# Kernel tuning notes

Measured on AMD Instinct MI355X. Metric: run time of the kernel, lower is better.

## Reference

```python
import jax, jax.numpy as jnp
import numpy as np

N, DIN, DOUT, R, E = 100000, 128, 256, 4, 600000
EPS = 1e-12


def setup_inputs() -> dict:
    key = jax.random.key(0)
    ks = jax.random.split(key, 8)
    x = jax.random.normal(ks[0], (N, DIN), dtype=jnp.float32)
    edge_index = jax.random.randint(ks[1], (R, 2, E), 0, N, dtype=jnp.int32)
    s1 = 1.0 / np.sqrt(DIN)
    s2 = 1.0 / np.sqrt(DOUT)
    W1n = jax.random.uniform(ks[2], (R, DOUT, DIN), jnp.float32, -s1, s1)
    W1r = jax.random.uniform(ks[3], (R, DOUT, DIN), jnp.float32, -s1, s1)
    b1 = jnp.zeros((R, DOUT), jnp.float32)
    W2n = jax.random.uniform(ks[4], (R, DOUT, DOUT), jnp.float32, -s2, s2)
    W2r = jax.random.uniform(ks[5], (R, DOUT, DOUT), jnp.float32, -s2, s2)
    b2 = jnp.zeros((R, DOUT), jnp.float32)
    return {"x": x, "edge_index": edge_index, "W1n": W1n, "b1": b1,
            "W1r": W1r, "W2n": W2n, "b2": b2, "W2r": W2r}


def _hetero_sage_layer(x, edge_index, Wn, b, Wr):
    # per-relation sum-aggregate of source features into destinations: [R, N, D]
    agg = jax.vmap(
        lambda e: jax.ops.segment_sum(x[e[0]], e[1], num_segments=N)
    )(edge_index)
    # SAGEConv: lin_l(agg) + bias + lin_r(x); mean across relations (to_hetero aggr='mean')
    out = (jnp.einsum('rnd,rod->rno', agg, Wn)
           + b[:, None, :]
           + jnp.einsum('nd,rod->rno', x, Wr))
    return out.mean(axis=0)  # [N, DOUT]


def _l2_normalize(h):
    nrm = jnp.sqrt(jnp.sum(h * h, axis=-1, keepdims=True))
    return h / jnp.maximum(nrm, EPS)


def reference(x, edge_index, W1n, b1, W1r, W2n, b2, W2r):
    h = _hetero_sage_layer(x, edge_index, W1n, b1, W1r)
    h = jax.nn.relu(_l2_normalize(h))  # dropout is identity in eval mode
    out = _hetero_sage_layer(h, edge_index, W2n, b2, W2r)
    return out  # x_dict['note']
```

## Files before the change

### kernel.cpp

```cpp
#include <hip/hip_runtime.h>
#include <hip/hip_bf16.h>

#define NN 100000
#define DIN 128
#define DOUT 256
#define RR 4
#define EE 600000
#define NB (RR * NN)
#define SCAN_BLKS 400
#define SCAN_CHUNK 1000
#define PBLKS 2048

typedef __attribute__((ext_vector_type(4))) float f32x4;
typedef __attribute__((ext_vector_type(8))) short short8;
typedef __attribute__((ext_vector_type(2))) uint uint2v;

__device__ __forceinline__ float bf2f(ushort u) {
    union { unsigned int i; float f; } v; v.i = ((unsigned int)u) << 16; return v.f;
}
__device__ __forceinline__ ushort f2bf(float f) {
    union { float f; unsigned int i; } v; v.f = f;
    unsigned int r = v.i + 0x7fff + ((v.i >> 16) & 1);
    return (ushort)(r >> 16);
}

__device__ __forceinline__ void ld_g2l16(const void* g, void* l) {
    __builtin_amdgcn_global_load_lds(
        (const __attribute__((address_space(1))) void*)g,
        (__attribute__((address_space(3))) void*)l, 16, 0, 0);
}

__device__ __forceinline__ void store_w(ushort* W, int kd, int o, float s) {
    int cs = ((kd >> 3) & 7) ^ (o & 7);
    W[((size_t)(kd >> 6) * 256 + o) * 64 + cs * 8 + (kd & 7)] = f2bf(s);
}

#define W1ELEMS (5 * 128 * 256)
#define W2ELEMS (5 * 256 * 256)
__global__ void wprep_all(const float* __restrict__ W1n, const float* __restrict__ W1r,
                          const float* __restrict__ W2n, const float* __restrict__ W2r,
                          const float* __restrict__ b1, const float* __restrict__ b2,
                          ushort* __restrict__ W1c, ushort* __restrict__ W2c,
                          float* __restrict__ b1s, float* __restrict__ b2s) {
    int idx = blockIdx.x * blockDim.x + threadIdx.x;
    if (idx < W1ELEMS) {
        int p = idx / (128 * 256), rem = idx - p * (128 * 256);
        int k = rem >> 8, o = rem & 255;
        float s;
        if (p == 0) {
            s = 0.f;
            for (int r = 0; r < RR; ++r) s += W1r[(size_t)r * DOUT * DIN + (long)o * DIN + k];
        } else {
            s = W1n[(size_t)(p - 1) * DOUT * DIN + (long)o * DIN + k];
        }
        store_w(W1c, p * 128 + k, o, s * 0.25f);
        return;
    }
    idx -= W1ELEMS;
    if (idx < W2ELEMS) {
        int p = idx / (256 * 256), rem = idx - p * (256 * 256);
        int k = rem >> 8, o = rem & 255;
        float s;
        if (p == 0) {
            s = 0.f;
            for (int r = 0; r < RR; ++r) s += W2r[(size_t)r * DOUT * DOUT + (long)o * DOUT + k];
        } else {
            s = W2n[(size_t)(p - 1) * DOUT * DOUT + (long)o * DOUT + k];
        }
        store_w(W2c, p * 256 + k, o, s * 0.25f);
        return;
    }
    idx -= W2ELEMS;
    if (idx < 512) {
        int o = idx & 255;
        const float* b = (idx < 256) ? b1 : b2;
        float s = 0.f;
        for (int r = 0; r < RR; ++r) s += b[(long)r * 256 + o];
        ((idx < 256) ? b1s : b2s)[o] = s * 0.25f;
    }
}

__global__ __launch_bounds__(256) void deg_count(const int* __restrict__ ei,
                                                 int* __restrict__ deg) {
    const int CH = EE / 4;
    int p = blockIdx.x & 7;
    const int stride = (PBLKS / 8) * 256;
    for (int idx = (blockIdx.x >> 3) * 256 + threadIdx.x; idx < RR * CH; idx += stride) {
        int r = idx / CH, j = idx - r * CH;
        int4 d = ((const int4*)(ei + (size_t)r * 2 * EE + EE))[j];
        if (((d.x >> 8) & 7) == p) atomicAdd(&deg[r * NN + d.x], 1);
        if (((d.y >> 8) & 7) == p) atomicAdd(&deg[r * NN + d.y], 1);
        if (((d.z >> 8) & 7) == p) atomicAdd(&deg[r * NN + d.z], 1);
        if (((d.w >> 8) & 7) == p) atomicAdd(&deg[r * NN + d.w], 1);
    }
}

__global__ __launch_bounds__(256) void fill_csr(const int* __restrict__ ei,
                                                int* __restrict__ cursor,
                                                int* __restrict__ elist) {
    const int CH = EE / 4;
    int p = blockIdx.x & 7;
    const int stride = (PBLKS / 8) * 256;
    for (int idx = (blockIdx.x >> 3) * 256 + threadIdx.x; idx < RR * CH; idx += stride) {
        int r = idx / CH, j = idx - r * CH;
        int4 d = ((const int4*)(ei + (size_t)r * 2 * EE + EE))[j];
        int4 s = ((const int4*)(ei + (size_t)r * 2 * EE))[j];
        if (((d.x >> 8) & 7) == p) elist[atomicAdd(&cursor[r * NN + d.x], 1)] = s.x;
        if (((d.y >> 8) & 7) == p) elist[atomicAdd(&cursor[r * NN + d.y], 1)] = s.y;
        if (((d.z >> 8) & 7) == p) elist[atomicAdd(&cursor[r * NN + d.z], 1)] = s.z;
        if (((d.w >> 8) & 7) == p) elist[atomicAdd(&cursor[r * NN + d.w], 1)] = s.w;
    }
}

__global__ __launch_bounds__(256) void scan_part(const int* __restrict__ deg,
                                                 int* __restrict__ bsum) {
    int b = blockIdx.x, t = threadIdx.x;
    int s = 0;
    for (int i = t; i < SCAN_CHUNK; i += 256) s += deg[b * SCAN_CHUNK + i];
    for (int o = 32; o > 0; o >>= 1) s += __shfl_down(s, o);
    __shared__ int red[4];
    if ((t & 63) == 0) red[t >> 6] = s;
    __syncthreads();
    if (t == 0) bsum[b] = red[0] + red[1] + red[2] + red[3];
}

__global__ __launch_bounds__(512) void scan_top(int* __restrict__ bsum) {
    __shared__ int v[512];
    int t = threadIdx.x;
    v[t] = (t < SCAN_BLKS) ? bsum[t] : 0;
    __syncthreads();
    for (int st = 1; st < 512; st <<= 1) {
        int tmp = (t >= st) ? v[t - st] : 0;
        __syncthreads();
        v[t] += tmp;
        __syncthreads();
    }
    if (t < SCAN_BLKS) bsum[t] = (t == 0) ? 0 : v[t - 1];
}

__global__ __launch_bounds__(256) void scan_final(int* __restrict__ degc,
                                                  const int* __restrict__ bsum,
                                                  int* __restrict__ off) {
    __shared__ int lv[1024];
    __shared__ int ts[256];
    int b = blockIdx.x, t = threadIdx.x;
    for (int i = t; i < 1024; i += 256)
        lv[i] = (i < SCAN_CHUNK) ? degc[b * SCAN_CHUNK + i] : 0;
    __syncthreads();
    int i0 = t * 4;
    int v0 = lv[i0], v1 = lv[i0 + 1], v2 = lv[i0 + 2], v3 = lv[i0 + 3];
    ts[t] = v0 + v1 + v2 + v3;
    __syncthreads();
    for (int st = 1; st < 256; st <<= 1) {
        int tmp = (t >= st) ? ts[t - st] : 0;
        __syncthreads();
        ts[t] += tmp;
        __syncthreads();
    }
    int run = bsum[b] + (t ? ts[t - 1] : 0);
    if (i0 < SCAN_CHUNK) {
        int base = b * SCAN_CHUNK + i0;
        off[base + 0] = run; degc[base + 0] = run; run += v0;
        off[base + 1] = run; degc[base + 1] = run; run += v1;
        off[base + 2] = run; degc[base + 2] = run; run += v2;
        off[base + 3] = run; degc[base + 3] = run; run += v3;
    }
    if (b == SCAN_BLKS - 1 && t == 255) off[NB] = bsum[b] + ts[255];
}

__global__ void cvt_x(const float* __restrict__ x, ushort* __restrict__ XB) {
    int t = blockIdx.x * blockDim.x + threadIdx.x;
    if (t >= NN * 32) return;
    int n = t >> 5, c4 = (t & 31) * 4;
    float4 v = *(const float4*)&x[(size_t)n * 128 + c4];
    ushort4 o = {f2bf(v.x), f2bf(v.y), f2bf(v.z), f2bf(v.w)};
    *(ushort4*)&XB[(size_t)n * 128 + c4] = o;
}

template <int D>
__global__ void gather_bf16(const ushort* __restrict__ feat,
                            const int* __restrict__ elist, const int* __restrict__ off,
                            ushort* __restrict__ agg, int sout, int chunk) {
    constexpr int V = D / 64;
    int wv = blockIdx.x * 4 + (threadIdx.x >> 6);
    int lane = threadIdx.x & 63;
    if (wv >= NN * chunk) return;
    int n = wv / chunk, rl = wv - n * chunk;
    int b = rl * NN + n;
    int beg = __builtin_amdgcn_readfirstlane(off[b]);
    int end = __builtin_amdgcn_readfirstlane(off[b + 1]);
    float acc[V];
#pragma unroll
    for (int v = 0; v < V; ++v) acc[v] = 0.f;
    const ushort* fbase = feat + lane * V;
    int e = beg;
    for (; e + 4 <= end; e += 4) {
        int s0 = elist[e], s1 = elist[e + 1], s2 = elist[e + 2], s3 = elist[e + 3];
        if constexpr (V == 2) {
            ushort2 a0 = *(const ushort2*)(fbase + (size_t)s0 * D);
            ushort2 a1 = *(const ushort2*)(fbase + (size_t)s1 * D);
            ushort2 a2 = *(const ushort2*)(fbase + (size_t)s2 * D);
            ushort2 a3 = *(const ushort2*)(fbase + (size_t)s3 * D);
            acc[0] += (bf2f(a0.x) + bf2f(a1.x)) + (bf2f(a2.x) + bf2f(a3.x));
            acc[1] += (bf2f(a0.y) + bf2f(a1.y)) + (bf2f(a2.y) + bf2f(a3.y));
        } else {
            ushort4 a0 = *(const ushort4*)(fbase + (size_t)s0 * D);
            ushort4 a1 = *(const ushort4*)(fbase + (size_t)s1 * D);
            ushort4 a2 = *(const ushort4*)(fbase + (size_t)s2 * D);
            ushort4 a3 = *(const ushort4*)(fbase + (size_t)s3 * D);
            acc[0] += (bf2f(a0.x) + bf2f(a1.x)) + (bf2f(a2.x) + bf2f(a3.x));
            acc[1] += (bf2f(a0.y) + bf2f(a1.y)) + (bf2f(a2.y) + bf2f(a3.y));
            acc[2] += (bf2f(a0.z) + bf2f(a1.z)) + (bf2f(a2.z) + bf2f(a3.z));
            acc[3] += (bf2f(a0.w) + bf2f(a1.w)) + (bf2f(a2.w) + bf2f(a3.w));
        }
    }
    for (; e < end; ++e) {
        int s0 = elist[e];
        if constexpr (V == 2) {
            ushort2 a = *(const ushort2*)(fbase + (size_t)s0 * D);
            acc[0] += bf2f(a.x); acc[1] += bf2f(a.y);
        } else {
            ushort4 a = *(const ushort4*)(fbase + (size_t)s0 * D);
            acc[0] += bf2f(a.x); acc[1] += bf2f(a.y);
            acc[2] += bf2f(a.z); acc[3] += bf2f(a.w);
        }
    }
    ushort* op = agg + (size_t)n * sout + rl * D + lane * V;
    if constexpr (V == 2) {
        uint u = (uint)f2bf(acc[0]) | ((uint)f2bf(acc[1]) << 16);
        *(uint*)op = u;
    } else {
        uint2v u;
        u.x = (uint)f2bf(acc[0]) | ((uint)f2bf(acc[1]) << 16);
        u.y = (uint)f2bf(acc[2]) | ((uint)f2bf(acc[3]) << 16);
        *(uint2v*)op = u;
    }
}

template <int MODE>
__global__ __launch_bounds__(256, 2) void gemm_fused(
    const ushort* __restrict__ F, int ldf, int K1,
    const ushort* __restrict__ G, int ldg, int K2,
    const ushort* __restrict__ W, const float* __restrict__ bias,
    void* __restrict__ Cout, int M) {
    __shared__ ushort lA[128 * 64];
    __shared__ ushort lB[256 * 64];
    const int tid = threadIdx.x;
    const int w = tid >> 6, lane = tid & 63;
    const int row0 = blockIdx.x * 128;

    f32x4 acc[8][4];
#pragma unroll
    for (int i = 0; i < 8; ++i)
#pragma unroll
        for (int j = 0; j < 4; ++j) acc[i][j] = {0.f, 0.f, 0.f, 0.f};

    const int arow = lane >> 3;
    const int asrc = ((lane & 7) ^ arow) << 3;
    const int ldst = lane * 8;
    const ushort* aF[4]; const ushort* aG[4];
#pragma unroll
    for (int c = 0; c < 4; ++c) {
        int rg = row0 + w * 32 + c * 8 + arow;
        if (rg > M - 1) rg = M - 1;
        aF[c] = F + (size_t)rg * ldf + asrc;
        aG[c] = G + (size_t)rg * ldg + asrc;
    }
    const int nt = (K1 + K2) >> 6;

    for (int t = 0; t < nt; ++t) {
        __syncthreads();
        int kb = t << 6;
#pragma unroll
        for (int c = 0; c < 4; ++c) {
            const ushort* src = (kb < K1) ? (aF[c] + kb) : (aG[c] + (kb - K1));
            ld_g2l16(src, &lA[(w * 32 + c * 8) * 64 + ldst]);
        }
        const ushort* wb = W + (size_t)t * (256 * 64);
#pragma unroll
        for (int c = 0; c < 8; ++c)
            ld_g2l16(wb + (w * 64 + c * 8) * 64 + ldst, &lB[(w * 64 + c * 8) * 64 + ldst]);
        asm volatile("s_waitcnt vmcnt(0)" ::: "memory");
        __syncthreads();
        __builtin_amdgcn_s_setprio(1);
#pragma unroll
        for (int ks = 0; ks < 2; ++ks) {
            const int co = (((ks * 4 + (lane >> 4)) ^ (lane & 7)) << 3);
            short8 af[8];
#pragma unroll
            for (int rf = 0; rf < 8; ++rf)
                af[rf] = *(const short8*)&lA[(rf * 16 + (lane & 15)) * 64 + co];
#pragma unroll
            for (int cf = 0; cf < 4; ++cf) {
                short8 bf8 = *(const short8*)&lB[(w * 64 + cf * 16 + (lane & 15)) * 64 + co];
#pragma unroll
                for (int rf = 0; rf < 8; ++rf)
                    acc[rf][cf] = __builtin_amdgcn_mfma_f32_16x16x32_bf16(
                        af[rf], bf8, acc[rf][cf], 0, 0, 0);
            }
        }
        __builtin_amdgcn_s_setprio(0);
    }

#pragma unroll
    for (int cf = 0; cf < 4; ++cf) {
        float badd = bias[w * 64 + cf * 16 + (lane & 15)];
#pragma unroll
        for (int rf = 0; rf < 8; ++rf)
#pragma unroll
            for (int m = 0; m < 4; ++m) acc[rf][cf][m] += badd;
    }

    if constexpr (MODE == 0) {
        float* Cf = (float*)Cout;
#pragma unroll
        for (int cf = 0; cf < 4; ++cf) {
            int col = w * 64 + cf * 16 + (lane & 15);
#pragma unroll
            for (int rf = 0; rf < 8; ++rf)
#pragma unroll
                for (int m = 0; m < 4; ++m) {
                    int r = row0 + rf * 16 + (lane >> 4) * 4 + m;
                    if (r < M)
                        __builtin_nontemporal_store(acc[rf][cf][m],
                                                    &Cf[(size_t)r * 256 + col]);
                }
        }
    } else {
        float* rs = (float*)lA;
        float ss[8][4];
#pragma unroll
        for (int rf = 0; rf < 8; ++rf)
#pragma unroll
            for (int m = 0; m < 4; ++m) {
                float s = 0.f;
#pragma unroll
                for (int cf = 0; cf < 4; ++cf) s += acc[rf][cf][m] * acc[rf][cf][m];
#pragma unroll
                for (int o = 1; o < 16; o <<= 1) s += __shfl_xor(s, o);
                ss[rf][m] = s;
            }
        __syncthreads();
        if ((lane & 15) == 0) {
#pragma unroll
            for (int rf = 0; rf < 8; ++rf)
#pragma unroll
                for (int m = 0; m < 4; ++m)
                    rs[w * 128 + rf * 16 + (lane >> 4) * 4 + m] = ss[rf][m];
        }
        __syncthreads();
        uint* HBw = (uint*)Cout;
#pragma unroll
        for (int rf = 0; rf < 8; ++rf)
#pragma unroll
            for (int m = 0; m < 4; ++m) {
                int tr = rf * 16 + (lane >> 4) * 4 + m;
                float tot = rs[tr] + rs[128 + tr] + rs[256 + tr] + rs[384 + tr];
                float inv = 1.0f / fmaxf(sqrtf(tot), 1e-12f);
                int r = row0 + tr;
#pragma unroll
                for (int cf = 0; cf < 4; ++cf) {
                    float v = fmaxf(acc[rf][cf][m] * inv, 0.f);
                    uint u = f2bf(v);
                    uint pu = __shfl_xor(u, 1);
                    if (!(lane & 1) && r < M)
                        HBw[(size_t)r * 128 + ((w * 64 + cf * 16 + (lane & 15)) >> 1)] =
                            u | (pu << 16);
                }
            }
    }
}

extern "C" void kernel_launch(void* const* d_in, const int* in_sizes, int n_in,
                              void* d_out, int out_size, void* d_ws, size_t ws_size,
                              hipStream_t stream) {
    const float* x   = (const float*)d_in[0];
    const int*   ei  = (const int*)d_in[1];
    const float* W1n = (const float*)d_in[2];
    const float* b1  = (const float*)d_in[3];
    const float* W1r = (const float*)d_in[4];
    const float* W2n = (const float*)d_in[5];
    const float* b2  = (const float*)d_in[6];
    const float* W2r = (const float*)d_in[7];

    ushort* HB  = (ushort*)d_ws;
    ushort* G1  = HB + (size_t)NN * 256;
    ushort* G2  = G1 + (size_t)NN * 512;
    ushort* XB  = G2;
    int* elist  = (int*)(G2 + (size_t)NN * 1024);
    int* degc   = elist + (size_t)RR * EE;
    int* off    = degc + NB;
    int* bsum   = off + NB + 1;
    ushort* W1c = (ushort*)(bsum + 512);
    ushort* W2c = W1c + 640 * 256;
    float* b1s  = (float*)(W2c + 1280 * 256);
    float* b2s  = b1s + 256;

    hipMemsetAsync(degc, 0, (size_t)NB * sizeof(int), stream);
    deg_count<<<PBLKS, 256, 0, stream>>>(ei, degc);
    scan_part<<<SCAN_BLKS, 256, 0, stream>>>(degc, bsum);
    scan_top<<<1, 512, 0, stream>>>(bsum);
    scan_final<<<SCAN_BLKS, 256, 0, stream>>>(degc, bsum, off);
    fill_csr<<<PBLKS, 256, 0, stream>>>(ei, degc, elist);

    {
        int total = W1ELEMS + W2ELEMS + 512;
        wprep_all<<<(total + 255) / 256, 256, 0, stream>>>(W1n, W1r, W2n, W2r, b1, b2,
                                                           W1c, W2c, b1s, b2s);
    }
    cvt_x<<<(NN * 32 + 255) / 256, 256, 0, stream>>>(x, XB);

    const int ggrid = (NN + 127) / 128;

    gather_bf16<128><<<NN, 256, 0, stream>>>(XB, elist, off, G1, 512, RR);
    gemm_fused<1><<<ggrid, 256, 0, stream>>>(XB, 128, 128, G1, 512, 512, W1c, b1s, HB, NN);

    gather_bf16<256><<<NN, 256, 0, stream>>>(HB, elist, off, G2, 1024, RR);
    gemm_fused<0><<<ggrid, 256, 0, stream>>>(HB, 256, 256, G2, 1024, 1024, W2c, b2s,
                                             d_out, NN);
}
```

Measured before the change: 718.5 us.

## Double-buffer LDS tiles and use 8-wave 2x4 warp grid in fused GEMM

```diff
diff --git a/kernel.cpp b/kernel.cpp
--- a/kernel.cpp
+++ b/kernel.cpp
@@ -45,7 +45,7 @@
     int idx = blockIdx.x * blockDim.x + threadIdx.x;
     if (idx < W1ELEMS) {
         int p = idx / (128 * 256), rem = idx - p * (128 * 256);
-        int k = rem >> 8, o = rem & 255;
+        int k = rem & 127, o = rem >> 7;
         float s;
         if (p == 0) {
             s = 0.f;
@@ -59,7 +59,7 @@
     idx -= W1ELEMS;
     if (idx < W2ELEMS) {
         int p = idx / (256 * 256), rem = idx - p * (256 * 256);
-        int k = rem >> 8, o = rem & 255;
+        int k = rem & 255, o = rem >> 8;
         float s;
         if (p == 0) {
             s = 0.f;
@@ -238,75 +238,86 @@
 }
 
 template <int MODE>
-__global__ __launch_bounds__(256, 2) void gemm_fused(
+__global__ __launch_bounds__(512, 2) void gemm_fused(
     const ushort* __restrict__ F, int ldf, int K1,
     const ushort* __restrict__ G, int ldg, int K2,
     const ushort* __restrict__ W, const float* __restrict__ bias,
     void* __restrict__ Cout, int M) {
-    __shared__ ushort lA[128 * 64];
-    __shared__ ushort lB[256 * 64];
+    __shared__ ushort lA[2][128 * 64];
+    __shared__ ushort lB[2][256 * 64];
     const int tid = threadIdx.x;
     const int w = tid >> 6, lane = tid & 63;
+    const int wr = w >> 2, wc = w & 3;
     const int row0 = blockIdx.x * 128;
 
-    f32x4 acc[8][4];
-#pragma unroll
-    for (int i = 0; i < 8; ++i)
+    f32x4 acc[4][4];
+#pragma unroll
+    for (int i = 0; i < 4; ++i)
 #pragma unroll
         for (int j = 0; j < 4; ++j) acc[i][j] = {0.f, 0.f, 0.f, 0.f};
 
     const int arow = lane >> 3;
     const int asrc = ((lane & 7) ^ arow) << 3;
     const int ldst = lane * 8;
-    const ushort* aF[4]; const ushort* aG[4];
-#pragma unroll
-    for (int c = 0; c < 4; ++c) {
-        int rg = row0 + w * 32 + c * 8 + arow;
+    const ushort* aF[2]; const ushort* aG[2];
+#pragma unroll
+    for (int c = 0; c < 2; ++c) {
+        int rg = row0 + w * 16 + c * 8 + arow;
         if (rg > M - 1) rg = M - 1;
         aF[c] = F + (size_t)rg * ldf + asrc;
         aG[c] = G + (size_t)rg * ldg + asrc;
     }
     const int nt = (K1 + K2) >> 6;
 
+    auto STAGE = [&](int buf, int t) {
+        int kb = t << 6;
+#pragma unroll
+        for (int c = 0; c < 2; ++c) {
+            const ushort* src = (kb < K1) ? (aF[c] + kb) : (aG[c] + (kb - K1));
+            ld_g2l16(src, &lA[buf][(w * 16 + c * 8) * 64 + ldst]);
+        }
+        const ushort* wb = W + (size_t)t * (256 * 64);
+#pragma unroll
+        for (int c = 0; c < 4; ++c)
+            ld_g2l16(wb + (w * 32 + c * 8) * 64 + ldst,
+                     &lB[buf][(w * 32 + c * 8) * 64 + ldst]);
+    };
+
+    STAGE(0, 0);
+    __syncthreads();
+
+    int cur = 0;
     for (int t = 0; t < nt; ++t) {
-        __syncthreads();
-        int kb = t << 6;
-#pragma unroll
-        for (int c = 0; c < 4; ++c) {
-            const ushort* src = (kb < K1) ? (aF[c] + kb) : (aG[c] + (kb - K1));
-            ld_g2l16(src, &lA[(w * 32 + c * 8) * 64 + ldst]);
-        }
-        const ushort* wb = W + (size_t)t * (256 * 64);
-#pragma unroll
-        for (int c = 0; c < 8; ++c)
-            ld_g2l16(wb + (w * 64 + c * 8) * 64 + ldst, &lB[(w * 64 + c * 8) * 64 + ldst]);
-        asm volatile("s_waitcnt vmcnt(0)" ::: "memory");
-        __syncthreads();
+        if (t + 1 < nt) STAGE(cur ^ 1, t + 1);
         __builtin_amdgcn_s_setprio(1);
 #pragma unroll
         for (int ks = 0; ks < 2; ++ks) {
             const int co = (((ks * 4 + (lane >> 4)) ^ (lane & 7)) << 3);
-            short8 af[8];
-#pragma unroll
-            for (int rf = 0; rf < 8; ++rf)
-                af[rf] = *(const short8*)&lA[(rf * 16 + (lane & 15)) * 64 + co];
+            short8 af[4];
+#pragma unroll
+            for (int rf = 0; rf < 4; ++rf)
+                af[rf] = *(const short8*)&lA[cur]
+                             [(wr * 64 + rf * 16 + (lane & 15)) * 64 + co];
 #pragma unroll
             for (int cf = 0; cf < 4; ++cf) {
-                short8 bf8 = *(const short8*)&lB[(w * 64 + cf * 16 + (lane & 15)) * 64 + co];
-#pragma unroll
-                for (int rf = 0; rf < 8; ++rf)
+                short8 bf8 = *(const short8*)&lB[cur]
+                                 [(wc * 64 + cf * 16 + (lane & 15)) * 64 + co];
+#pragma unroll
+                for (int rf = 0; rf < 4; ++rf)
                     acc[rf][cf] = __builtin_amdgcn_mfma_f32_16x16x32_bf16(
                         af[rf], bf8, acc[rf][cf], 0, 0, 0);
             }
         }
         __builtin_amdgcn_s_setprio(0);
+        __syncthreads();
+        cur ^= 1;
     }
 
 #pragma unroll
     for (int cf = 0; cf < 4; ++cf) {
-        float badd = bias[w * 64 + cf * 16 + (lane & 15)];
-#pragma unroll
-        for (int rf = 0; rf < 8; ++rf)
+        float badd = bias[wc * 64 + cf * 16 + (lane & 15)];
+#pragma unroll
+        for (int rf = 0; rf < 4; ++rf)
 #pragma unroll
             for (int m = 0; m < 4; ++m) acc[rf][cf][m] += badd;
     }
@@ -315,22 +326,22 @@
         float* Cf = (float*)Cout;
 #pragma unroll
         for (int cf = 0; cf < 4; ++cf) {
-            int col = w * 64 + cf * 16 + (lane & 15);
-#pragma unroll
-            for (int rf = 0; rf < 8; ++rf)
+            int col = wc * 64 + cf * 16 + (lane & 15);
+#pragma unroll
+            for (int rf = 0; rf < 4; ++rf)
 #pragma unroll
                 for (int m = 0; m < 4; ++m) {
-                    int r = row0 + rf * 16 + (lane >> 4) * 4 + m;
+                    int r = row0 + wr * 64 + rf * 16 + (lane >> 4) * 4 + m;
                     if (r < M)
                         __builtin_nontemporal_store(acc[rf][cf][m],
                                                     &Cf[(size_t)r * 256 + col]);
                 }
         }
     } else {
-        float* rs = (float*)lA;
-        float ss[8][4];
-#pragma unroll
-        for (int rf = 0; rf < 8; ++rf)
+        float* rs = (float*)&lA[0][0];
+        float ss[4][4];
+#pragma unroll
+        for (int rf = 0; rf < 4; ++rf)
 #pragma unroll
             for (int m = 0; m < 4; ++m) {
                 float s = 0.f;
@@ -340,21 +351,20 @@
                 for (int o = 1; o < 16; o <<= 1) s += __shfl_xor(s, o);
                 ss[rf][m] = s;
             }
-        __syncthreads();
         if ((lane & 15) == 0) {
 #pragma unroll
-            for (int rf = 0; rf < 8; ++rf)
+            for (int rf = 0; rf < 4; ++rf)
 #pragma unroll
                 for (int m = 0; m < 4; ++m)
-                    rs[w * 128 + rf * 16 + (lane >> 4) * 4 + m] = ss[rf][m];
+                    rs[wc * 128 + wr * 64 + rf * 16 + (lane >> 4) * 4 + m] = ss[rf][m];
         }
         __syncthreads();
         uint* HBw = (uint*)Cout;
 #pragma unroll
-        for (int rf = 0; rf < 8; ++rf)
+        for (int rf = 0; rf < 4; ++rf)
 #pragma unroll
             for (int m = 0; m < 4; ++m) {
-                int tr = rf * 16 + (lane >> 4) * 4 + m;
+                int tr = wr * 64 + rf * 16 + (lane >> 4) * 4 + m;
                 float tot = rs[tr] + rs[128 + tr] + rs[256 + tr] + rs[384 + tr];
                 float inv = 1.0f / fmaxf(sqrtf(tot), 1e-12f);
                 int r = row0 + tr;
@@ -364,7 +374,7 @@
                     uint u = f2bf(v);
                     uint pu = __shfl_xor(u, 1);
                     if (!(lane & 1) && r < M)
-                        HBw[(size_t)r * 128 + ((w * 64 + cf * 16 + (lane & 15)) >> 1)] =
+                        HBw[(size_t)r * 128 + ((wc * 64 + cf * 16 + (lane & 15)) >> 1)] =
                             u | (pu << 16);
                 }
             }
@@ -413,9 +423,9 @@
     const int ggrid = (NN + 127) / 128;
 
     gather_bf16<128><<<NN, 256, 0, stream>>>(XB, elist, off, G1, 512, RR);
-    gemm_fused<1><<<ggrid, 256, 0, stream>>>(XB, 128, 128, G1, 512, 512, W1c, b1s, HB, NN);
+    gemm_fused<1><<<ggrid, 512, 0, stream>>>(XB, 128, 128, G1, 512, 512, W1c, b1s, HB, NN);
 
     gather_bf16<256><<<NN, 256, 0, stream>>>(HB, elist, off, G2, 1024, RR);
-    gemm_fused<0><<<ggrid, 256, 0, stream>>>(HB, 256, 256, G2, 1024, 1024, W2c, b2s,
+    gemm_fused<0><<<ggrid, 512, 0, stream>>>(HB, 256, 256, G2, 1024, 1024, W2c, b2s,
                                              d_out, NN);
 }
```

New measurement: 776.4 us. 1.08x slower.
